# Kernel tuning notes

Measured on AMD Instinct MI355X. Metric: run time of the kernel, lower is better.

## Reference

```python
import jax, jax.numpy as jnp
import numpy as np

B, S, D = 8, 2048, 512


def setup_inputs() -> dict:
    key = jax.random.key(0)
    ks = jax.random.split(key, 11)
    scale = 1.0 / np.sqrt(D)
    inp = {"x": jax.random.normal(ks[0], (B, S, D), dtype=jnp.float32)}
    names = ["q", "k", "v", "g", "o"]
    for i, n in enumerate(names):
        inp[f"W{n}"] = jax.random.normal(ks[1 + 2 * i], (D, D), dtype=jnp.float32) * scale
        inp[f"b{n}"] = jax.random.normal(ks[2 + 2 * i], (D,), dtype=jnp.float32) * 0.01
    return inp


def reference(x, Wq, bq, Wk, bk, Wv, bv, Wg, bg, Wo, bo):
    # Projections (torch nn.Linear: x @ W.T + b)
    Q = x @ Wq.T + bq            # (B,S,D)
    K = x @ Wk.T + bk
    V = x @ Wv.T + bv
    gamma = jax.nn.sigmoid(x @ Wg.T + bg)

    # Recurrent linear-attention scan over time.
    # State St: (B,D,D); update: St = gamma_t[:, :, None] * St + k_t ⊗ v_t
    # (decay broadcasts along the key/row dimension, matching
    #  gamma_i.transpose(1,2) * S in the torch code)
    def step(St, qkvg):
        q_t, k_t, v_t, g_t = qkvg           # each (B,D)
        St = g_t[:, :, None] * St + k_t[:, :, None] * v_t[:, None, :]
        out_t = jnp.einsum('bd,bde->be', q_t, St)  # q_i @ S
        return St, out_t

    S0 = jnp.zeros((B, D, D), dtype=x.dtype)
    # time-major inputs for scan: (S,B,D)
    seq = (Q.transpose(1, 0, 2), K.transpose(1, 0, 2),
           V.transpose(1, 0, 2), gamma.transpose(1, 0, 2))
    _, outs = jax.lax.scan(step, S0, seq)   # outs: (S,B,D)
    O = outs.transpose(1, 0, 2)             # (B,S,D)
    return O @ Wo.T + bo
```

## Files before the change

kernel.cpp:

```cpp
#include <hip/hip_runtime.h>
#include <hip/hip_bf16.h>
#include <stdint.h>


#define B_ 8
#define S_ 2048
#define D_ 512
#define M_ (B_ * S_)
#define NSUB 64
#define SUBL 32
#define NSUP 8
#define SUPL 256

typedef __bf16 bf16x8 __attribute__((ext_vector_type(8)));
typedef float f32x4 __attribute__((ext_vector_type(4)));

__device__ __forceinline__ float bflo(uint32_t u){ return __uint_as_float(u<<16); }
__device__ __forceinline__ float bfhi(uint32_t u){ return __uint_as_float(u&0xffff0000u); }
__device__ __forceinline__ uint16_t f2bf(float f){
    uint32_t u = __float_as_uint(f);
    return (uint16_t)((u + 0x7fffu + ((u>>16)&1u)) >> 16);
}
__device__ __forceinline__ uint32_t pack2bf(float a, float b){
    return (uint32_t)f2bf(a) | ((uint32_t)f2bf(b)<<16);
}
__device__ __forceinline__ void gload16(const void* g, void* l){
    __builtin_amdgcn_global_load_lds(
        (const __attribute__((address_space(1))) uint32_t*)g,
        (__attribute__((address_space(3))) uint32_t*)l, 16, 0, 0);
}

__global__ __launch_bounds__(256) void convall(const float* __restrict__ x,
                                               const float* w0, const float* w1,
                                               const float* w2, const float* w3,
                                               const float* w4,
                                               uint16_t* __restrict__ xb,
                                               uint16_t* __restrict__ Wb){
    const int id = blockIdx.x;
    const float* in;
    uint16_t* out;
    size_t i;
    if (id < 4096) {
        in = x; out = xb;
        i = ((size_t)id*256 + threadIdx.x)*8;
    } else {
        const float* ws[5] = {w0,w1,w2,w3,w4};
        const int wid = (id - 4096) >> 7, off = (id - 4096) & 127;
        in = ws[wid]; out = Wb + (size_t)wid*D_*D_;
        i = ((size_t)off*256 + threadIdx.x)*8;
    }
    float4 a = *(const float4*)&in[i];
    float4 b = *(const float4*)&in[i+4];
    uint4 o; o.x=pack2bf(a.x,a.y); o.y=pack2bf(a.z,a.w); o.z=pack2bf(b.x,b.y); o.w=pack2bf(b.z,b.w);
    *(uint4*)&out[i] = o;
}

__global__ __launch_bounds__(256) void proj4(const uint16_t* __restrict__ A,
                                             const uint16_t* __restrict__ Wb,
                                             const float* __restrict__ bq_,
                                             const float* __restrict__ bk_,
                                             const float* __restrict__ bv_,
                                             const float* __restrict__ bg_,
                                             uint16_t* __restrict__ Qb,
                                             uint16_t* __restrict__ Kb,
                                             uint16_t* __restrict__ VT,
                                             uint16_t* __restrict__ Gb)
{
    __shared__ __attribute__((aligned(16))) uint16_t SM[2][16384];
    const int tid = threadIdx.x, wave = tid>>6, lane = tid&63;
    const int m0 = blockIdx.x*128, n0 = blockIdx.y*128;
    const int wr = (wave>>1)*64, wc = (wave&1)*64;
    const int fr = lane&15, fq = lane>>4;
    const int sect = blockIdx.y >> 2;
    const int n0c = n0 & 511;
    f32x4 acc[4][4] = {};

    auto STAGE = [&](int kt, int p){
        const int k0 = kt*64;
#pragma unroll
        for (int i = 0; i < 4; ++i) {
            const int c = i*256 + tid;
            const int row = c>>3, kc = ((c&7) ^ (row&7))*8;
            const int ldsb = (i*256 + wave*64)*8;
            gload16(&A [(size_t)(m0+row)*D_ + k0 + kc], &SM[p][ldsb]);
            gload16(&Wb[(size_t)(n0+row)*D_ + k0 + kc], &SM[p][8192+ldsb]);
        }
    };
    auto COMP = [&](int p){
#pragma unroll
        for (int kk = 0; kk < 64; kk += 32) {
            const int sc = (kk + fq*8) ^ ((fr&7)<<3);
            bf16x8 af[4], bfv[4];
#pragma unroll
            for (int m = 0; m < 4; ++m) af[m]  = *(const bf16x8*)&SM[p][(wr+m*16+fr)*64 + sc];
#pragma unroll
            for (int n = 0; n < 4; ++n) bfv[n] = *(const bf16x8*)&SM[p][8192+(wc+n*16+fr)*64 + sc];
            if (sect == 2) {
#pragma unroll
                for (int m = 0; m < 4; ++m)
#pragma unroll
                    for (int n = 0; n < 4; ++n)
                        acc[m][n] = __builtin_amdgcn_mfma_f32_16x16x32_bf16(bfv[n], af[m], acc[m][n], 0,0,0);
            } else {
#pragma unroll
                for (int m = 0; m < 4; ++m)
#pragma unroll
                    for (int n = 0; n < 4; ++n)
                        acc[m][n] = __builtin_amdgcn_mfma_f32_16x16x32_bf16(af[m], bfv[n], acc[m][n], 0,0,0);
            }
        }
    };

    STAGE(0, 0);
    __syncthreads();
    int p = 0;
    for (int kt = 0; kt < 8; ++kt) {
        if (kt < 7) STAGE(kt+1, p^1);
        COMP(p);
        __syncthreads();
        p ^= 1;
    }

    uint16_t (*L)[136] = (uint16_t(*)[136])&SM[0][0];
    const float* bias = (sect==0) ? bq_ : (sect==1) ? bk_ : (sect==2) ? bv_ : bg_;
    if (sect == 2) {
#pragma unroll
        for (int n = 0; n < 4; ++n)
#pragma unroll
            for (int q = 0; q < 4; ++q) {
                const int dvl = wc + n*16 + fq*4 + q;
                const float bvv = bias[n0c + dvl];
#pragma unroll
                for (int m = 0; m < 4; ++m)
                    L[dvl][wr + m*16 + fr] = f2bf(acc[m][n][q] + bvv);
            }
    } else {
#pragma unroll
        for (int n = 0; n < 4; ++n) {
            const int cl = wc + n*16 + fr;
            const float bvv = bias[n0c + cl];
#pragma unroll
            for (int m = 0; m < 4; ++m)
#pragma unroll
                for (int q = 0; q < 4; ++q) {
                    float c = acc[m][n][q] + bvv;
                    if (sect == 3) c = 1.f/(1.f + expf(-c));
                    L[wr + m*16 + fq*4 + q][cl] = f2bf(c);
                }
        }
    }
    __syncthreads();
    const int bb = m0 >> 11, t0 = m0 & 2047;
#pragma unroll
    for (int it = 0; it < 8; ++it) {
        const int r = it*16 + (tid>>4), c8 = (tid&15)*8;
        uint4 v = *(uint4*)&L[r][c8];
        if (sect == 0)      *(uint4*)&Qb[(size_t)(m0+r)*D_ + n0c + c8] = v;
        else if (sect == 1) *(uint4*)&Kb[(size_t)(m0+r)*D_ + n0c + c8] = v;
        else if (sect == 3) *(uint4*)&Gb[(size_t)(m0+r)*D_ + n0c + c8] = v;
        else                *(uint4*)&VT[((size_t)bb*D_ + n0c + r)*S_ + t0 + c8] = v;
    }
}

__global__ __launch_bounds__(256) void mfma_gemm(const uint16_t* __restrict__ A,
                                                 const uint16_t* __restrict__ Wt,
                                                 const float* __restrict__ bias,
                                                 float* __restrict__ out)
{
    __shared__ __attribute__((aligned(16))) uint16_t SM[2][16384];
    const int tid = threadIdx.x, wave = tid>>6, lane = tid&63;
    const int m0 = blockIdx.x*128, n0 = blockIdx.y*128;
    const int wr = (wave>>1)*64, wc = (wave&1)*64;
    const int fr = lane&15, fq = lane>>4;
    f32x4 acc[4][4] = {};

    auto STAGE = [&](int kt, int p){
        const int k0 = kt*64;
#pragma unroll
        for (int i = 0; i < 4; ++i) {
            const int c = i*256 + tid;
            const int row = c>>3, kc = ((c&7) ^ (row&7))*8;
            const int ldsb = (i*256 + wave*64)*8;
            gload16(&A [(size_t)(m0+row)*D_ + k0 + kc], &SM[p][ldsb]);
            gload16(&Wt[(size_t)(n0+row)*D_ + k0 + kc], &SM[p][8192+ldsb]);
        }
    };
    auto COMP = [&](int p){
#pragma unroll
        for (int kk = 0; kk < 64; kk += 32) {
            const int sc = (kk + fq*8) ^ ((fr&7)<<3);
            bf16x8 af[4], bfv[4];
#pragma unroll
            for (int m = 0; m < 4; ++m) af[m]  = *(const bf16x8*)&SM[p][(wr+m*16+fr)*64 + sc];
#pragma unroll
            for (int n = 0; n < 4; ++n) bfv[n] = *(const bf16x8*)&SM[p][8192+(wc+n*16+fr)*64 + sc];
#pragma unroll
            for (int m = 0; m < 4; ++m)
#pragma unroll
                for (int n = 0; n < 4; ++n)
                    acc[m][n] = __builtin_amdgcn_mfma_f32_16x16x32_bf16(af[m], bfv[n], acc[m][n], 0,0,0);
        }
    };

    STAGE(0, 0);
    __syncthreads();
    int p = 0;
    for (int kt = 0; kt < 8; ++kt) {
        if (kt < 7) STAGE(kt+1, p^1);
        COMP(p);
        __syncthreads();
        p ^= 1;
    }

    float (*L32)[68] = (float(*)[68])&SM[0][0];
#pragma unroll
    for (int h = 0; h < 2; ++h) {
        if (wc == h*64) {
#pragma unroll
            for (int n = 0; n < 4; ++n) {
                const float bvv = bias[n0 + wc + n*16 + fr];
#pragma unroll
                for (int m = 0; m < 4; ++m)
#pragma unroll
                    for (int q = 0; q < 4; ++q)
                        L32[wr + m*16 + fq*4 + q][n*16 + fr] = acc[m][n][q] + bvv;
            }
        }
        __syncthreads();
#pragma unroll
        for (int it = 0; it < 8; ++it) {
            const int r = it*16 + (tid>>4), c4 = (tid&15)*4;
            *(uint4*)&out[(size_t)(m0+r)*D_ + n0 + h*64 + c4] = *(uint4*)&L32[r][c4];
        }
        __syncthreads();
    }
}

__global__ __launch_bounds__(256) void prep(const uint16_t* __restrict__ Gb,
                                            uint16_t* __restrict__ Qb,
                                            uint16_t* __restrict__ Kb,
                                            uint16_t* __restrict__ KT,
                                            float* __restrict__ T)
{
    const int sub = blockIdx.x, b = blockIdx.y;
    const int tid = threadIdx.x;
    const int dk0 = tid*2;
    const size_t rowbase = ((size_t)b*S_ + sub*SUBL)*D_;
    const uint16_t* gp = Gb + rowbase + dk0;
    uint16_t*       qp = Qb + rowbase + dk0;
    uint16_t*       kp = Kb + rowbase + dk0;

    float mu0 = 1.f, mu1 = 1.f;
    uint32_t ksave[SUBL];
#pragma unroll
    for (int t = 0; t < SUBL; ++t) {
        const uint32_t g2 = *(const uint32_t*)(gp + (size_t)t*D_);
        const uint32_t qu = *(const uint32_t*)(qp + (size_t)t*D_);
        const uint32_t ku = *(const uint32_t*)(kp + (size_t)t*D_);
        mu0 = fmaxf(mu0*bflo(g2), 1e-30f);
        mu1 = fmaxf(mu1*bfhi(g2), 1e-30f);
        const float r0 = __builtin_amdgcn_rcpf(mu0);
        const float r1 = __builtin_amdgcn_rcpf(mu1);
        *(uint32_t*)(qp + (size_t)t*D_) = pack2bf(bflo(qu)*mu0, bfhi(qu)*mu1);
        const uint32_t kw = pack2bf(bflo(ku)*r0, bfhi(ku)*r1);
        *(uint32_t*)(kp + (size_t)t*D_) = kw;
        ksave[t] = kw;
    }
    T[((size_t)b*NSUB + sub)*D_ + dk0]     = mu0;
    T[((size_t)b*NSUB + sub)*D_ + dk0 + 1] = mu1;

    uint16_t* d0 = &KT[((size_t)b*D_ + dk0)*S_ + sub*SUBL];
    uint16_t* d1 = d0 + S_;
#pragma unroll
    for (int q4 = 0; q4 < 4; ++q4) {
        uint4 lo, hi;
        lo.x = (ksave[q4*8+0]&0xffffu) | (ksave[q4*8+1]<<16);
        lo.y = (ksave[q4*8+2]&0xffffu) | (ksave[q4*8+3]<<16);
        lo.z = (ksave[q4*8+4]&0xffffu) | (ksave[q4*8+5]<<16);
        lo.w = (ksave[q4*8+6]&0xffffu) | (ksave[q4*8+7]<<16);
        hi.x = (ksave[q4*8+0]>>16) | (ksave[q4*8+1]&0xffff0000u);
        hi.y = (ksave[q4*8+2]>>16) | (ksave[q4*8+3]&0xffff0000u);
        hi.z = (ksave[q4*8+4]>>16) | (ksave[q4*8+5]&0xffff0000u);
        hi.w = (ksave[q4*8+6]>>16) | (ksave[q4*8+7]&0xffff0000u);
        *(uint4*)&d0[q4*8] = lo;
        *(uint4*)&d1[q4*8] = hi;
    }
}

__global__ __launch_bounds__(512) void tables(const float* __restrict__ T,
                                              float* __restrict__ Pre,
                                              float* __restrict__ Suf,
                                              float* __restrict__ Lam)
{
    const int sp = blockIdx.x, b = blockIdx.y, dk = threadIdx.x;
    float run = 1.f;
#pragma unroll
    for (int m = 0; m < 8; ++m) {
        Pre[((size_t)b*NSUB + sp*8+m)*D_ + dk] = run;
        run *= T[((size_t)b*NSUB + sp*8+m)*D_ + dk];
    }
    Lam[((size_t)b*NSUP + sp)*D_ + dk] = run;
    float rs = 1.f;
#pragma unroll
    for (int m = 7; m >= 0; --m) {
        rs *= T[((size_t)b*NSUB + sp*8+m)*D_ + dk];
        Suf[((size_t)b*NSUB + sp*8+m)*D_ + dk] = rs;
    }
}

__device__ __forceinline__ int swz(int r, int c){ return r*D_ + (c ^ ((r&7)<<3)); }

__global__ __launch_bounds__(256) void pairsA(const uint16_t* __restrict__ Qt,
                                              const uint16_t* __restrict__ Kh,
                                              const float* __restrict__ T,
                                              uint16_t* __restrict__ P)
{
    __shared__ __attribute__((aligned(16))) uint16_t qs[SUBL*D_];
    __shared__ __attribute__((aligned(16))) uint16_t ks[SUBL*D_];
    __shared__ float D_lds[D_];
    const int idx = blockIdx.x, sp = blockIdx.y, b = blockIdx.z;
    int i = 0;
    while (((i+1)*(i+2))/2 <= idx) ++i;
    const int j = idx - (i*(i+1))/2;

    const int tid = threadIdx.x, wave = tid>>6, lane = tid&63;
    const int fr = lane&15, fq = lane>>4;
    const int mq = wave>>1, nq = wave&1;
    const size_t qrow = (size_t)b*S_ + sp*SUPL + i*SUBL;
    const size_t krow = (size_t)b*S_ + sp*SUPL + j*SUBL;
    const size_t prow = ((size_t)(b*NSUP + sp)*SUPL + i*SUBL);

#pragma unroll
    for (int z = 0; z < 8; ++z) {
        int ch = z*256 + tid, r = ch>>6, c = (ch&63)*8;
        *(uint4*)&qs[swz(r,c)] = *(const uint4*)&Qt[(qrow + r)*D_ + c];
    }
    const int dkA = tid*2, dkB = tid*2+1;
    float d0 = 1.f, d1 = 1.f;
    for (int m = j; m < i; ++m) {
        d0 *= T[((size_t)b*NSUB + sp*8 + m)*D_ + dkA];
        d1 *= T[((size_t)b*NSUB + sp*8 + m)*D_ + dkB];
    }
    D_lds[dkA] = d0; D_lds[dkB] = d1;
    __syncthreads();

#pragma unroll
    for (int z = 0; z < 8; ++z) {
        int ch = z*256 + tid, r = ch>>6, c = (ch&63)*8;
        uint4 u = *(const uint4*)&Kh[(krow + r)*D_ + c];
        uint4 o;
        o.x = pack2bf(bflo(u.x)*D_lds[c+0], bfhi(u.x)*D_lds[c+1]);
        o.y = pack2bf(bflo(u.y)*D_lds[c+2], bfhi(u.y)*D_lds[c+3]);
        o.z = pack2bf(bflo(u.z)*D_lds[c+4], bfhi(u.z)*D_lds[c+5]);
        o.w = pack2bf(bflo(u.w)*D_lds[c+6], bfhi(u.w)*D_lds[c+7]);
        *(uint4*)&ks[swz(r,c)] = o;
    }
    __syncthreads();

    f32x4 a0 = {}, a1 = {}, a2 = {}, a3 = {};
#pragma unroll
    for (int kk = 0; kk < 512; kk += 128) {
        bf16x8 q0 = *(const bf16x8*)&qs[swz(mq*16+fr, kk      + fq*8)];
        bf16x8 k0 = *(const bf16x8*)&ks[swz(nq*16+fr, kk      + fq*8)];
        bf16x8 q1 = *(const bf16x8*)&qs[swz(mq*16+fr, kk + 32 + fq*8)];
        bf16x8 k1 = *(const bf16x8*)&ks[swz(nq*16+fr, kk + 32 + fq*8)];
        bf16x8 q2 = *(const bf16x8*)&qs[swz(mq*16+fr, kk + 64 + fq*8)];
        bf16x8 k2 = *(const bf16x8*)&ks[swz(nq*16+fr, kk + 64 + fq*8)];
        bf16x8 q3 = *(const bf16x8*)&qs[swz(mq*16+fr, kk + 96 + fq*8)];
        bf16x8 k3 = *(const bf16x8*)&ks[swz(nq*16+fr, kk + 96 + fq*8)];
        a0 = __builtin_amdgcn_mfma_f32_16x16x32_bf16(q0, k0, a0, 0,0,0);
        a1 = __builtin_amdgcn_mfma_f32_16x16x32_bf16(q1, k1, a1, 0,0,0);
        a2 = __builtin_amdgcn_mfma_f32_16x16x32_bf16(q2, k2, a2, 0,0,0);
        a3 = __builtin_amdgcn_mfma_f32_16x16x32_bf16(q3, k3, a3, 0,0,0);
    }
    const int ul = nq*16 + fr;
#pragma unroll
    for (int q_ = 0; q_ < 4; ++q_) {
        const int tl = mq*16 + fq*4 + q_;
        float v = a0[q_] + a1[q_] + a2[q_] + a3[q_];
        if (i == j && ul > tl) v = 0.f;
        P[(prow + tl)*SUPL + j*SUBL + ul] = f2bf(v);
    }
}

__global__ __launch_bounds__(256) void dsgemm(const uint16_t* __restrict__ VT,
                                              const uint16_t* __restrict__ KT,
                                              const float* __restrict__ Suf,
                                              uint16_t* __restrict__ Sst)
{
    __shared__ __attribute__((aligned(16))) uint16_t As[2][128][40];
    __shared__ __attribute__((aligned(16))) uint16_t Bs[2][128][40];
    const int tile = blockIdx.x, c = blockIdx.y, b = blockIdx.z;
    const int m0 = (tile&3)*128, n0 = (tile>>2)*128;
    const int tid = threadIdx.x, wave = tid>>6, lane = tid&63;
    const int wr = (wave>>1)*64, wc = (wave&1)*64;
    const int fr = lane&15, fq = lane>>4;
    f32x4 acc[4][4] = {};

    auto STAGE = [&](int j, int p){
        const int t0 = c*SUPL + j*SUBL;
#pragma unroll
        for (int ch = tid; ch < 512; ch += 256) {
            int row = ch>>2, tc = (ch&3)*8;
            *(uint4*)&As[p][row][tc] = *(const uint4*)&VT[((size_t)b*D_ + m0+row)*S_ + t0 + tc];
        }
#pragma unroll
        for (int ch = tid; ch < 512; ch += 256) {
            int row = ch>>2, tc = (ch&3)*8;
            uint4 u = *(const uint4*)&KT[((size_t)b*D_ + n0+row)*S_ + t0 + tc];
            float sf = Suf[((size_t)b*NSUB + c*8 + j)*D_ + n0 + row];
            uint4 o;
            o.x = pack2bf(bflo(u.x)*sf, bfhi(u.x)*sf);
            o.y = pack2bf(bflo(u.y)*sf, bfhi(u.y)*sf);
            o.z = pack2bf(bflo(u.z)*sf, bfhi(u.z)*sf);
            o.w = pack2bf(bflo(u.w)*sf, bfhi(u.w)*sf);
            *(uint4*)&Bs[p][row][tc] = o;
        }
    };

    STAGE(0, 0);
    __syncthreads();
    int p = 0;
    for (int j = 0; j < 8; ++j) {
        if (j < 7) STAGE(j+1, p^1);
        bf16x8 af[4], bf[4];
#pragma unroll
        for (int m = 0; m < 4; ++m) af[m] = *(const bf16x8*)&As[p][wr+m*16+fr][fq*8];
#pragma unroll
        for (int n = 0; n < 4; ++n) bf[n] = *(const bf16x8*)&Bs[p][wc+n*16+fr][fq*8];
#pragma unroll
        for (int m = 0; m < 4; ++m)
#pragma unroll
            for (int n = 0; n < 4; ++n)
                acc[m][n] = __builtin_amdgcn_mfma_f32_16x16x32_bf16(af[m], bf[n], acc[m][n], 0,0,0);
        __syncthreads();
        p ^= 1;
    }
#pragma unroll
    for (int n = 0; n < 4; ++n) {
        const int dk = n0 + wc + n*16 + fr;
#pragma unroll
        for (int m = 0; m < 4; ++m)
#pragma unroll
            for (int q = 0; q < 4; ++q) {
                const int dv = m0 + wr + m*16 + fq*4 + q;
                Sst[(((size_t)c*B_ + b)*D_ + dv)*D_ + dk] = f2bf(acc[m][n][q]);
            }
    }
}

__global__ __launch_bounds__(256) void scanfix(uint16_t* __restrict__ Sst,
                                               const float* __restrict__ Lam)
{
    const int id = blockIdx.x*256 + threadIdx.x;
    const int g = id & 63, dv = (id>>6) & 511, b = id >> 15;
    const int dk = g*8;
    float s[8];
    {
        uint4 u = *(const uint4*)&Sst[(((size_t)0*B_ + b)*D_ + dv)*D_ + dk];
        s[0]=bflo(u.x); s[1]=bfhi(u.x); s[2]=bflo(u.y); s[3]=bfhi(u.y);
        s[4]=bflo(u.z); s[5]=bfhi(u.z); s[6]=bflo(u.w); s[7]=bfhi(u.w);
    }
    for (int c = 1; c < 7; ++c) {
        const size_t bs = (((size_t)c*B_ + b)*D_ + dv)*D_ + dk;
        uint4 d = *(const uint4*)&Sst[bs];
        float4 l0 = *(const float4*)&Lam[((size_t)b*NSUP + c)*D_ + dk];
        float4 l1 = *(const float4*)&Lam[((size_t)b*NSUP + c)*D_ + dk + 4];
        s[0] = l0.x*s[0] + bflo(d.x); s[1] = l0.y*s[1] + bfhi(d.x);
        s[2] = l0.z*s[2] + bflo(d.y); s[3] = l0.w*s[3] + bfhi(d.y);
        s[4] = l1.x*s[4] + bflo(d.z); s[5] = l1.y*s[5] + bfhi(d.z);
        s[6] = l1.z*s[6] + bflo(d.w); s[7] = l1.w*s[7] + bfhi(d.w);
        uint4 o;
        o.x = pack2bf(s[0],s[1]); o.y = pack2bf(s[2],s[3]);
        o.z = pack2bf(s[4],s[5]); o.w = pack2bf(s[6],s[7]);
        *(uint4*)&Sst[bs] = o;
    }
}

__global__ __launch_bounds__(256) void bigout(const uint16_t* __restrict__ Qt,
                                              const float* __restrict__ Pre,
                                              const uint16_t* __restrict__ Sst,
                                              const uint16_t* __restrict__ Pb,
                                              const uint16_t* __restrict__ VT,
                                              uint16_t* __restrict__ O)
{
    __shared__ __attribute__((aligned(16))) uint16_t SM[2][16384];
    __shared__ float PreL[4*512];
    const int m0 = blockIdx.x*128, n0 = blockIdx.y*128;
    const int b = blockIdx.z>>3, sp = blockIdx.z&7;
    const int tid = threadIdx.x, wave = tid>>6, lane = tid&63;
    const int wr = (wave>>1)*64, wc = (wave&1)*64;
    const int fr = lane&15, fq = lane>>4;
    const int i0 = m0>>5;

#pragma unroll
    for (int z = 0; z < 8; ++z) {
        int idx = z*256 + tid;
        PreL[idx] = Pre[((size_t)b*NSUB + sp*8 + i0 + (idx>>9))*D_ + (idx&511)];
    }
    f32x4 acc[4][4] = {};
    uint4 areg[4];

    auto ISSUE_A = [&](int kt){
        const int k0 = kt*64;
#pragma unroll
        for (int z = 0; z < 4; ++z) {
            int ch = z*256 + tid, r = ch>>3, cc = (ch&7)*8;
            areg[z] = *(const uint4*)&Qt[((size_t)b*S_ + sp*SUPL + m0 + r)*D_ + k0 + cc];
        }
    };
    auto WRITE_A = [&](int kt, int p){
        const int k0 = kt*64;
#pragma unroll
        for (int z = 0; z < 4; ++z) {
            int ch = z*256 + tid, r = ch>>3, cc = (ch&7)*8;
            const float* pr = &PreL[((r>>5)<<9) + k0 + cc];
            uint4 u = areg[z];
            uint4 o;
            o.x = pack2bf(bflo(u.x)*pr[0], bfhi(u.x)*pr[1]);
            o.y = pack2bf(bflo(u.y)*pr[2], bfhi(u.y)*pr[3]);
            o.z = pack2bf(bflo(u.z)*pr[4], bfhi(u.z)*pr[5]);
            o.w = pack2bf(bflo(u.w)*pr[6], bfhi(u.w)*pr[7]);
            *(uint4*)&SM[p][r*64 + (cc ^ ((r&7)<<3))] = o;
        }
    };
    auto STAGE_A_GL = [&](int kt, int p){
        const int u0 = (kt-8)*64;
#pragma unroll
        for (int z = 0; z < 4; ++z) {
            int ch = z*256 + tid, row = ch>>3, kc = ((ch&7) ^ (row&7))*8;
            int ldsb = (z*256 + wave*64)*8;
            gload16(&Pb[((size_t)(b*NSUP + sp)*SUPL + m0 + row)*SUPL + u0 + kc], &SM[p][ldsb]);
        }
    };
    auto STAGE_B = [&](int kt, int p){
        if (kt < 8) {
            const int k0 = kt*64;
#pragma unroll
            for (int z = 0; z < 4; ++z) {
                int ch = z*256 + tid, row = ch>>3, kc = ((ch&7) ^ (row&7))*8;
                int ldsb = (z*256 + wave*64)*8;
                gload16(&Sst[(((size_t)(sp-1)*B_ + b)*D_ + n0 + row)*D_ + k0 + kc], &SM[p][8192+ldsb]);
            }
        } else {
            const int u0 = (kt-8)*64;
#pragma unroll
            for (int z = 0; z < 4; ++z) {
                int ch = z*256 + tid, row = ch>>3, kc = ((ch&7) ^ (row&7))*8;
                int ldsb = (z*256 + wave*64)*8;
                gload16(&VT[((size_t)b*D_ + n0 + row)*S_ + sp*SUPL + u0 + kc], &SM[p][8192+ldsb]);
            }
        }
    };
    auto COMP = [&](int p, int kt){
        const bf16x8 zz = {};
#pragma unroll
        for (int kk = 0; kk < 64; kk += 32) {
            const int sc = (kk + fq*8) ^ ((fr&7)<<3);
            bf16x8 af[4], bfv[4];
#pragma unroll
            for (int m = 0; m < 4; ++m) af[m] = *(const bf16x8*)&SM[p][(wr+m*16+fr)*64 + sc];
            if (kt >= 8) {
                const int jb = ((kt-8)*64 + kk) >> 5;
#pragma unroll
                for (int m = 0; m < 4; ++m) {
                    const int ib = (m0 + wr + m*16) >> 5;
                    if (jb > ib) af[m] = zz;
                }
            }
#pragma unroll
            for (int n = 0; n < 4; ++n) bfv[n] = *(const bf16x8*)&SM[p][8192+(wc+n*16+fr)*64 + sc];
#pragma unroll
            for (int m = 0; m < 4; ++m)
#pragma unroll
                for (int n = 0; n < 4; ++n)
                    acc[m][n] = __builtin_amdgcn_mfma_f32_16x16x32_bf16(af[m], bfv[n], acc[m][n], 0,0,0);
        }
    };

    const int kt0 = (sp == 0) ? 8 : 0;
    if (kt0 < 8) {
        ISSUE_A(kt0);
        STAGE_B(kt0, 0);
        __syncthreads();
        WRITE_A(kt0, 0);
    } else {
        STAGE_A_GL(kt0, 0);
        STAGE_B(kt0, 0);
    }
    __syncthreads();

    int p = 0;
    for (int kt = kt0; kt < 12; ++kt) {
        const int nxt = kt + 1;
        if (nxt < 12) {
            if (nxt < 8) ISSUE_A(nxt); else STAGE_A_GL(nxt, p^1);
            STAGE_B(nxt, p^1);
        }
        COMP(p, kt);
        if (nxt < 12 && nxt < 8) WRITE_A(nxt, p^1);
        __syncthreads();
        p ^= 1;
    }

    uint16_t (*L)[136] = (uint16_t(*)[136])&SM[0][0];
#pragma unroll
    for (int n = 0; n < 4; ++n) {
        const int cl = wc + n*16 + fr;
#pragma unroll
        for (int m = 0; m < 4; ++m)
#pragma unroll
            for (int q = 0; q < 4; ++q)
                L[wr + m*16 + fq*4 + q][cl] = f2bf(acc[m][n][q]);
    }
    __syncthreads();
#pragma unroll
    for (int it = 0; it < 8; ++it) {
        const int r = it*16 + (tid>>4), c8 = (tid&15)*8;
        *(uint4*)&O[((size_t)b*S_ + sp*SUPL + m0 + r)*D_ + n0 + c8] = *(uint4*)&L[r][c8];
    }
}

extern "C" void kernel_launch(void* const* d_in, const int* in_sizes, int n_in,
                              void* d_out, int out_size, void* d_ws, size_t ws_size,
                              hipStream_t stream)
{
    (void)in_sizes; (void)n_in; (void)out_size; (void)ws_size;
    const float* x  = (const float*)d_in[0];
    const float* Wq = (const float*)d_in[1];  const float* bq = (const float*)d_in[2];
    const float* Wk = (const float*)d_in[3];  const float* bk = (const float*)d_in[4];
    const float* Wv = (const float*)d_in[5];  const float* bv = (const float*)d_in[6];
    const float* Wg = (const float*)d_in[7];  const float* bg = (const float*)d_in[8];
    const float* Wo = (const float*)d_in[9];  const float* bo = (const float*)d_in[10];

    char* w = (char*)d_ws;
    const size_t MD2 = (size_t)M_*D_*2;
    uint16_t* Wb = (uint16_t*)w;                       w += 5*(size_t)D_*D_*2;
    uint16_t* xb = (uint16_t*)w;                       w += MD2;
    uint16_t* Qb = (uint16_t*)w;                       w += MD2;
    uint16_t* Kb = (uint16_t*)w;                       w += MD2;
    uint16_t* KT = (uint16_t*)w;                       w += MD2;
    uint16_t* VT = (uint16_t*)w;                       w += MD2;
    uint16_t* Gb = (uint16_t*)w;                       w += MD2;
    uint16_t* Sst = (uint16_t*)w;                      w += (size_t)7*B_*D_*D_*2;
    uint16_t* Pb  = (uint16_t*)w;                      w += (size_t)B_*NSUP*SUPL*SUPL*2;
    float*    T   = (float*)w;                         w += (size_t)B_*NSUB*D_*4;
    float*    Pre = (float*)w;                         w += (size_t)B_*NSUB*D_*4;
    float*    Suf = (float*)w;                         w += (size_t)B_*NSUB*D_*4;
    float*    Lam = (float*)w;                         w += (size_t)B_*NSUP*D_*4;

    convall<<<dim3(4096 + 5*128), 256, 0, stream>>>(x, Wq, Wk, Wv, Wg, Wo, xb, Wb);

    proj4<<<dim3(M_/128, 16), 256, 0, stream>>>(xb, Wb, bq, bk, bv, bg, Qb, Kb, VT, Gb);

    prep<<<dim3(NSUB, B_), 256, 0, stream>>>(Gb, Qb, Kb, KT, T);
    tables<<<dim3(NSUP, B_), 512, 0, stream>>>(T, Pre, Suf, Lam);

    pairsA<<<dim3(36, NSUP, B_), 256, 0, stream>>>(Qb, Kb, T, Pb);
    dsgemm<<<dim3(16, 7, B_), 256, 0, stream>>>(VT, KT, Suf, Sst);
    scanfix<<<dim3(1024), 256, 0, stream>>>(Sst, Lam);

    bigout<<<dim3(2, 4, B_*NSUP), 256, 0, stream>>>(Qb, Pre, Sst, Pb, VT, xb);

    mfma_gemm<<<dim3(M_/128, D_/128), 256, 0, stream>>>(xb, Wb + 4*(size_t)D_*D_, bo, (float*)d_out);
}
```

Measured before the change: 200.2 us.

## Use 4-stage K32 LDS pipeline with explicit vmcnt waits in projection GEMM

Replaces the double-buffered K=64 staging in the QKVG projection kernel with a four-slot ring of K=32 tiles, keeping three loads in flight and using explicit s_waitcnt vmcnt counts plus raw barriers. The LDS swizzle is changed to fit the narrower 32-element rows. This aims to hide global-load latency better in the projection GEMM, at the cost of twice as many barriers per K step and hand-tuned wait counts that must match the number of outstanding loads.

```diff
diff --git a/kernel.cpp b/kernel.cpp
--- a/kernel.cpp
+++ b/kernel.cpp
@@ -66,62 +66,70 @@
                                              uint16_t* __restrict__ VT,
                                              uint16_t* __restrict__ Gb)
 {
-    __shared__ __attribute__((aligned(16))) uint16_t SM[2][16384];
+    __shared__ __attribute__((aligned(16))) uint16_t SM[32768];
     const int tid = threadIdx.x, wave = tid>>6, lane = tid&63;
     const int m0 = blockIdx.x*128, n0 = blockIdx.y*128;
     const int wr = (wave>>1)*64, wc = (wave&1)*64;
     const int fr = lane&15, fq = lane>>4;
     const int sect = blockIdx.y >> 2;
     const int n0c = n0 & 511;
+    const int rc = (fq ^ ((fr>>1)&3))*8;
     f32x4 acc[4][4] = {};
 
-    auto STAGE = [&](int kt, int p){
-        const int k0 = kt*64;
-#pragma unroll
-        for (int i = 0; i < 4; ++i) {
-            const int c = i*256 + tid;
-            const int row = c>>3, kc = ((c&7) ^ (row&7))*8;
-            const int ldsb = (i*256 + wave*64)*8;
-            gload16(&A [(size_t)(m0+row)*D_ + k0 + kc], &SM[p][ldsb]);
-            gload16(&Wb[(size_t)(n0+row)*D_ + k0 + kc], &SM[p][8192+ldsb]);
-        }
-    };
-    auto COMP = [&](int p){
-#pragma unroll
-        for (int kk = 0; kk < 64; kk += 32) {
-            const int sc = (kk + fq*8) ^ ((fr&7)<<3);
-            bf16x8 af[4], bfv[4];
-#pragma unroll
-            for (int m = 0; m < 4; ++m) af[m]  = *(const bf16x8*)&SM[p][(wr+m*16+fr)*64 + sc];
-#pragma unroll
-            for (int n = 0; n < 4; ++n) bfv[n] = *(const bf16x8*)&SM[p][8192+(wc+n*16+fr)*64 + sc];
-            if (sect == 2) {
-#pragma unroll
-                for (int m = 0; m < 4; ++m)
-#pragma unroll
-                    for (int n = 0; n < 4; ++n)
-                        acc[m][n] = __builtin_amdgcn_mfma_f32_16x16x32_bf16(bfv[n], af[m], acc[m][n], 0,0,0);
-            } else {
-#pragma unroll
-                for (int m = 0; m < 4; ++m)
-#pragma unroll
-                    for (int n = 0; n < 4; ++n)
-                        acc[m][n] = __builtin_amdgcn_mfma_f32_16x16x32_bf16(af[m], bfv[n], acc[m][n], 0,0,0);
-            }
-        }
-    };
-
-    STAGE(0, 0);
-    __syncthreads();
-    int p = 0;
-    for (int kt = 0; kt < 8; ++kt) {
-        if (kt < 7) STAGE(kt+1, p^1);
-        COMP(p);
-        __syncthreads();
-        p ^= 1;
-    }
-
-    uint16_t (*L)[136] = (uint16_t(*)[136])&SM[0][0];
+    auto STAGE = [&](int ct, int s){
+        const int k0 = ct*32;
+#pragma unroll
+        for (int z = 0; z < 2; ++z) {
+            const int ch  = z*256 + tid;
+            const int row = ch >> 2, sl = ch & 3;
+            const int kc  = (sl ^ ((row>>1)&3)) * 8;
+            const int ldsb = s*8192 + (z*256 + wave*64)*8;
+            gload16(&A [(size_t)(m0+row)*D_ + k0 + kc], &SM[ldsb]);
+            gload16(&Wb[(size_t)(n0+row)*D_ + k0 + kc], &SM[4096 + ldsb]);
+        }
+    };
+    auto COMP = [&](int s){
+        const int sb = s*8192;
+        bf16x8 af[4], bfv[4];
+#pragma unroll
+        for (int m = 0; m < 4; ++m) af[m]  = *(const bf16x8*)&SM[sb + (wr+m*16+fr)*32 + rc];
+#pragma unroll
+        for (int n = 0; n < 4; ++n) bfv[n] = *(const bf16x8*)&SM[sb + 4096 + (wc+n*16+fr)*32 + rc];
+        if (sect == 2) {
+#pragma unroll
+            for (int m = 0; m < 4; ++m)
+#pragma unroll
+                for (int n = 0; n < 4; ++n)
+                    acc[m][n] = __builtin_amdgcn_mfma_f32_16x16x32_bf16(bfv[n], af[m], acc[m][n], 0,0,0);
+        } else {
+#pragma unroll
+            for (int m = 0; m < 4; ++m)
+#pragma unroll
+                for (int n = 0; n < 4; ++n)
+                    acc[m][n] = __builtin_amdgcn_mfma_f32_16x16x32_bf16(af[m], bfv[n], acc[m][n], 0,0,0);
+        }
+    };
+
+    STAGE(0, 0); STAGE(1, 1); STAGE(2, 2);
+#pragma unroll 1
+    for (int i = 0; i < 16; ++i) {
+        if (i < 13) {
+            STAGE(i+3, (i+3)&3);
+            asm volatile("s_waitcnt vmcnt(12)" ::: "memory");
+        } else if (i == 13) {
+            asm volatile("s_waitcnt vmcnt(8)" ::: "memory");
+        } else if (i == 14) {
+            asm volatile("s_waitcnt vmcnt(4)" ::: "memory");
+        } else {
+            asm volatile("s_waitcnt vmcnt(0)" ::: "memory");
+        }
+        __builtin_amdgcn_s_barrier();
+        COMP(i & 3);
+        __builtin_amdgcn_s_barrier();
+    }
+    __syncthreads();
+
+    uint16_t (*L)[136] = (uint16_t(*)[136])&SM[0];
     const float* bias = (sect==0) ? bq_ : (sect==1) ? bk_ : (sect==2) ? bv_ : bg_;
     if (sect == 2) {
 #pragma unroll
```

Measured after the change: 212.3 us. 6.1% more time.
